# Optimization experiments

Measured on AMD Instinct MI355X. Metric: run time of the kernel, lower is better.

Reference implementation:

```python
import jax, jax.numpy as jnp
import numpy as np

V, E, H, T, B, NT = 50000, 100, 256, 128, 512, 20


def _gl(k, shape, fan):
    return jax.random.normal(k, shape, jnp.float32) * (1.0 / np.sqrt(fan))


def setup_inputs() -> dict:
    key = jax.random.key(0)
    ks = jax.random.split(key, 20)
    inp = {
        'word_inputs': jax.random.randint(ks[0], (B, T), 0, V),
        'word_seq_lengths': jnp.full((B,), T, dtype=jnp.int32),
        'char_inputs': jnp.zeros((B * T, 1), dtype=jnp.int32),
        'batch_label': jax.random.randint(ks[1], (B, T), 0, NT),
        'mask': jnp.ones((B, T), dtype=jnp.bool_),
        'embed': _gl(ks[2], (V, E), E).at[0].set(0.0),  # padding_idx=0
    }
    i = 3
    for d in ('f', 'b'):
        inp['Wih_' + d] = _gl(ks[i + 0], (4 * H, E), E)
        inp['Whh_' + d] = _gl(ks[i + 1], (4 * H, H), H)
        inp['bih_' + d] = jnp.zeros((4 * H,), jnp.float32)
        inp['bhh_' + d] = jnp.zeros((4 * H,), jnp.float32)
        inp['Q_' + d] = _gl(ks[i + 2], (H, E), H)  # mogrify round 1: x <- 2*sig(h Q) * x
        inp['R_' + d] = _gl(ks[i + 3], (E, H), E)  # mogrify round 2: h <- 2*sig(x R) * h
        i += 4
    inp['Wt'] = _gl(ks[i], (NT, 2 * H), 2 * H)
    inp['bt'] = jnp.zeros((NT,), jnp.float32)
    return inp


def _mog_lstm(xs, Wih, Whh, bih, bhh, Q, R):
    # xs: [T, B, E]; mog=2 Mogrifier rounds then standard LSTM cell (i,f,g,o order)
    def step(carry, xt):
        h, c = carry
        xm = 2.0 * jax.nn.sigmoid(h @ Q) * xt
        hm = 2.0 * jax.nn.sigmoid(xm @ R) * h
        g = xm @ Wih.T + hm @ Whh.T + (bih + bhh)
        gi, gf, gg, go = jnp.split(g, 4, axis=-1)
        c = jax.nn.sigmoid(gf) * c + jax.nn.sigmoid(gi) * jnp.tanh(gg)
        h = jax.nn.sigmoid(go) * jnp.tanh(c)
        return (h, c), h
    h0 = jnp.zeros((xs.shape[1], H), xs.dtype)
    _, hs = jax.lax.scan(step, (h0, h0), xs)
    return hs  # [T, B, H]


def reference(word_inputs, word_seq_lengths, char_inputs, batch_label, mask,
              embed, Wih_f, Whh_f, bih_f, bhh_f, Q_f, R_f,
              Wih_b, Whh_b, bih_b, bhh_b, Q_b, R_b, Wt, bt):
    x = embed[word_inputs]                       # [B, T, E]; dropout = identity (eval)
    xs = jnp.transpose(x, (1, 0, 2))             # [T, B, E]
    hf = _mog_lstm(xs, Wih_f, Whh_f, bih_f, bhh_f, Q_f, R_f)
    hb = _mog_lstm(xs[::-1], Wih_b, Whh_b, bih_b, bhh_b, Q_b, R_b)[::-1]
    feat = jnp.concatenate([hf, hb], axis=-1)    # [T, B, 2H]
    logits = feat @ Wt.T + bt                    # [T, B, NT]
    tag_seq = jnp.argmax(logits, axis=-1).T      # [B, T]
    return mask.astype(tag_seq.dtype) * tag_seq
```

## Files before the change

kernel.cpp:

```cpp
#include <hip/hip_runtime.h>
#include <math.h>

#define TT 128
#define BB 512
#define EE 100
#define HH 256
#define G4 1024
#define NTAG 20
#define NCH 92
#define PW3SZ (NCH * 4096)
#define QP2SZ (16 * 1600)
#define RP3SZ (7 * 4096)

__device__ __forceinline__ float sigm(float x) { return 1.0f / (1.0f + expf(-x)); }

__global__ void prep7(const float* __restrict__ Wih, const float* __restrict__ Whh,
                      const float* __restrict__ bih, const float* __restrict__ bhh,
                      const float* __restrict__ Q, const float* __restrict__ R,
                      float* __restrict__ PW3, float* __restrict__ QP2,
                      float* __restrict__ RP3, float* __restrict__ bP)
{
    int idx = blockIdx.x * blockDim.x + threadIdx.x;
    if (idx < PW3SZ) {
        int chunk = idx >> 12, rem = idx & 4095;
        int n = rem >> 2, kk = rem & 3;
        int k = chunk * 4 + kk;
        PW3[idx] = (k < EE) ? Wih[n * EE + k]
                 : (k < EE + HH) ? Whh[n * HH + (k - EE)] : 0.f;
    } else if (idx < PW3SZ + QP2SZ) {
        int i = idx - PW3SZ;
        int kqb = i / 1600, rem = i - kqb * 1600;
        int e = rem >> 4, q = (rem >> 2) & 3, kk = rem & 3;
        int k = (kqb * 4 + q) * 4 + kk;
        QP2[i] = Q[k * EE + e];
    } else if (idx < PW3SZ + QP2SZ + RP3SZ) {
        int i = idx - (PW3SZ + QP2SZ);
        int kqb = i >> 12, rem = i & 4095;
        int j = rem >> 4, q = (rem >> 2) & 3, kk = rem & 3;
        int k = (kqb * 4 + q) * 4 + kk;
        RP3[i] = (k < EE) ? R[k * HH + j] : 0.f;
    } else if (idx < PW3SZ + QP2SZ + RP3SZ + G4) {
        int n = idx - (PW3SZ + QP2SZ + RP3SZ);
        bP[n] = bih[n] + bhh[n];
    }
}

#define P3L(S, c) { const int cc_ = ((c) <= 45) ? (c) : 45; \
    const float* wp_ = PWd + (size_t)(cbase + cc_) * 4096 + n0 * 4; \
    W##S##0 = *(const float4*)(wp_);      W##S##1 = *(const float4*)(wp_ + 4); \
    W##S##2 = *(const float4*)(wp_ + 8);  W##S##3 = *(const float4*)(wp_ + 12); \
    const float* xp_ = sAT + (cbase + cc_) * 16; \
    X##S##0 = *(const float4*)(xp_);      X##S##1 = *(const float4*)(xp_ + 4); \
    X##S##2 = *(const float4*)(xp_ + 8);  X##S##3 = *(const float4*)(xp_ + 12); }

#define P3F(S) { \
    a00 += (X##S##0).x*(W##S##0).x + (X##S##1).x*(W##S##0).y + (X##S##2).x*(W##S##0).z + (X##S##3).x*(W##S##0).w; \
    a01 += (X##S##0).x*(W##S##1).x + (X##S##1).x*(W##S##1).y + (X##S##2).x*(W##S##1).z + (X##S##3).x*(W##S##1).w; \
    a02 += (X##S##0).x*(W##S##2).x + (X##S##1).x*(W##S##2).y + (X##S##2).x*(W##S##2).z + (X##S##3).x*(W##S##2).w; \
    a03 += (X##S##0).x*(W##S##3).x + (X##S##1).x*(W##S##3).y + (X##S##2).x*(W##S##3).z + (X##S##3).x*(W##S##3).w; \
    a10 += (X##S##0).y*(W##S##0).x + (X##S##1).y*(W##S##0).y + (X##S##2).y*(W##S##0).z + (X##S##3).y*(W##S##0).w; \
    a11 += (X##S##0).y*(W##S##1).x + (X##S##1).y*(W##S##1).y + (X##S##2).y*(W##S##1).z + (X##S##3).y*(W##S##1).w; \
    a12 += (X##S##0).y*(W##S##2).x + (X##S##1).y*(W##S##2).y + (X##S##2).y*(W##S##2).z + (X##S##3).y*(W##S##2).w; \
    a13 += (X##S##0).y*(W##S##3).x + (X##S##1).y*(W##S##3).y + (X##S##2).y*(W##S##3).z + (X##S##3).y*(W##S##3).w; \
    a20 += (X##S##0).z*(W##S##0).x + (X##S##1).z*(W##S##0).y + (X##S##2).z*(W##S##0).z + (X##S##3).z*(W##S##0).w; \
    a21 += (X##S##0).z*(W##S##1).x + (X##S##1).z*(W##S##1).y + (X##S##2).z*(W##S##1).z + (X##S##3).z*(W##S##1).w; \
    a22 += (X##S##0).z*(W##S##2).x + (X##S##1).z*(W##S##2).y + (X##S##2).z*(W##S##2).z + (X##S##3).z*(W##S##2).w; \
    a23 += (X##S##0).z*(W##S##3).x + (X##S##1).z*(W##S##3).y + (X##S##2).z*(W##S##3).z + (X##S##3).z*(W##S##3).w; \
    a30 += (X##S##0).w*(W##S##0).x + (X##S##1).w*(W##S##0).y + (X##S##2).w*(W##S##0).z + (X##S##3).w*(W##S##0).w; \
    a31 += (X##S##0).w*(W##S##1).x + (X##S##1).w*(W##S##1).y + (X##S##2).w*(W##S##1).z + (X##S##3).w*(W##S##1).w; \
    a32 += (X##S##0).w*(W##S##2).x + (X##S##1).w*(W##S##2).y + (X##S##2).w*(W##S##2).z + (X##S##3).w*(W##S##2).w; \
    a33 += (X##S##0).w*(W##S##3).x + (X##S##1).w*(W##S##3).y + (X##S##2).w*(W##S##3).z + (X##S##3).w*(W##S##3).w; }

__global__ __launch_bounds__(512, 1) void lstm7(
    const int* __restrict__ words, const float* __restrict__ embed,
    const float* __restrict__ QPf, const float* __restrict__ RPf,
    const float* __restrict__ PWf, const float* __restrict__ bPf,
    const float* __restrict__ QPb, const float* __restrict__ RPb,
    const float* __restrict__ PWb, const float* __restrict__ bPb,
    float* hfbuf, float* hbbuf)
{
    const int bid = blockIdx.x;
    const int dir = bid & 1;
    const int cb  = bid >> 1;
    const int b0  = cb * 4;
    const int tid = threadIdx.x;

    const float* QPd = dir ? QPb : QPf;
    const float* RPd = dir ? RPb : RPf;
    const float* PWd = dir ? PWb : PWf;
    const float* bP  = dir ? bPb : bPf;
    float* hout = dir ? hbbuf : hfbuf;

    __shared__ alignas(16) float sAT[368 * 4];
    __shared__ alignas(16) float sAlin[4 * 112];
    __shared__ alignas(16) float sH[4 * HH];
    __shared__ alignas(16) float sG[2 * 4 * G4];
    __shared__ int sWords[4 * TT];

    const int e  = tid & 127;
    const int r1 = tid >> 7;
    const int j2  = tid & 255;
    const int r20 = (tid >> 8) * 2, r21 = r20 + 1;
    const int n0    = (tid & 255) * 4;
    const int g3    = tid >> 8;
    const int cbase = g3 * 46;
    const int j4  = tid & 255;
    const int r4a = (tid >> 8) * 2, r4b = r4a + 1;
    float c0 = 0.f, c1 = 0.f;

    const float4 bvr = *(const float4*)(bP + n0);
    const float4 bv  = (g3 == 0) ? bvr : make_float4(0.f, 0.f, 0.f, 0.f);

    sWords[tid & 511] = words[(b0 + (tid >> 7)) * TT + (tid & 127)];
    if (tid < 48)  sAT[(356 + (tid >> 2)) * 4 + (tid & 3)] = 0.f;
    if (tid >= 64 && tid < 112) {
        const int i = tid - 64, r = i / 12, p = i - r * 12;
        sAlin[r * 112 + 100 + p] = 0.f;
    }
    __syncthreads();

    for (int s = 0; s < TT; ++s) {
        const int t = dir ? (TT - 1 - s) : s;

        if (e < EE) {
            const int w = sWords[r1 * TT + t];
            const float x = __builtin_nontemporal_load(&embed[(size_t)w * EE + e]);
            if (s == 0) {
                sAT[e * 4 + r1] = x;
                sAlin[r1 * 112 + e] = x;
            } else {
                float ac0 = 0.f, ac1 = 0.f, ac2 = 0.f, ac3 = 0.f;
                const float* hp0 = sH + r1 * HH;
                #pragma unroll
                for (int kqb = 0; kqb < 16; ++kqb) {
                    const float* qp = QPd + kqb * 1600 + e * 16;
                    const float4 q0 = *(const float4*)(qp);
                    const float4 q1 = *(const float4*)(qp + 4);
                    const float4 q2 = *(const float4*)(qp + 8);
                    const float4 q3 = *(const float4*)(qp + 12);
                    const float4 h0 = *(const float4*)(hp0 + kqb * 16);
                    const float4 h1 = *(const float4*)(hp0 + kqb * 16 + 4);
                    const float4 h2 = *(const float4*)(hp0 + kqb * 16 + 8);
                    const float4 h3 = *(const float4*)(hp0 + kqb * 16 + 12);
                    ac0 += h0.x*q0.x + h0.y*q0.y + h0.z*q0.z + h0.w*q0.w;
                    ac1 += h1.x*q1.x + h1.y*q1.y + h1.z*q1.z + h1.w*q1.w;
                    ac2 += h2.x*q2.x + h2.y*q2.y + h2.z*q2.z + h2.w*q2.w;
                    ac3 += h3.x*q3.x + h3.y*q3.y + h3.z*q3.z + h3.w*q3.w;
                }
                const float xm = 2.f * sigm((ac0 + ac1) + (ac2 + ac3)) * x;
                sAT[e * 4 + r1] = xm;
                sAlin[r1 * 112 + e] = xm;
            }
        }
        __syncthreads();

        if (s == 0) {
            sAT[(100 + j2) * 4 + r20] = 0.f;
            sAT[(100 + j2) * 4 + r21] = 0.f;
        } else {
            float s0a = 0.f, s0b = 0.f, s1a = 0.f, s1b = 0.f;
            const float* x0p = sAlin + r20 * 112;
            const float* x1p = sAlin + r21 * 112;
            #pragma unroll
            for (int kqb = 0; kqb < 7; ++kqb) {
                const float* rp = RPd + kqb * 4096 + j2 * 16;
                const float4 w0 = *(const float4*)(rp);
                const float4 w1 = *(const float4*)(rp + 4);
                const float4 w2 = *(const float4*)(rp + 8);
                const float4 w3 = *(const float4*)(rp + 12);
                const float4 xa0 = *(const float4*)(x0p + kqb * 16);
                const float4 xa1 = *(const float4*)(x0p + kqb * 16 + 4);
                const float4 xa2 = *(const float4*)(x0p + kqb * 16 + 8);
                const float4 xa3 = *(const float4*)(x0p + kqb * 16 + 12);
                const float4 xb0 = *(const float4*)(x1p + kqb * 16);
                const float4 xb1 = *(const float4*)(x1p + kqb * 16 + 4);
                const float4 xb2 = *(const float4*)(x1p + kqb * 16 + 8);
                const float4 xb3 = *(const float4*)(x1p + kqb * 16 + 12);
                s0a += xa0.x*w0.x + xa0.y*w0.y + xa0.z*w0.z + xa0.w*w0.w;
                s0b += xa1.x*w1.x + xa1.y*w1.y + xa1.z*w1.z + xa1.w*w1.w;
                s0a += xa2.x*w2.x + xa2.y*w2.y + xa2.z*w2.z + xa2.w*w2.w;
                s0b += xa3.x*w3.x + xa3.y*w3.y + xa3.z*w3.z + xa3.w*w3.w;
                s1a += xb0.x*w0.x + xb0.y*w0.y + xb0.z*w0.z + xb0.w*w0.w;
                s1b += xb1.x*w1.x + xb1.y*w1.y + xb1.z*w1.z + xb1.w*w1.w;
                s1a += xb2.x*w2.x + xb2.y*w2.y + xb2.z*w2.z + xb2.w*w2.w;
                s1b += xb3.x*w3.x + xb3.y*w3.y + xb3.z*w3.z + xb3.w*w3.w;
            }
            sAT[(100 + j2) * 4 + r20] = 2.f * sigm(s0a + s0b) * sH[r20 * HH + j2];
            sAT[(100 + j2) * 4 + r21] = 2.f * sigm(s1a + s1b) * sH[r21 * HH + j2];
        }
        __syncthreads();

        {
            float a00=bv.x,a01=bv.y,a02=bv.z,a03=bv.w;
            float a10=bv.x,a11=bv.y,a12=bv.z,a13=bv.w;
            float a20=bv.x,a21=bv.y,a22=bv.z,a23=bv.w;
            float a30=bv.x,a31=bv.y,a32=bv.z,a33=bv.w;
            float4 WA0,WA1,WA2,WA3,XA0,XA1,XA2,XA3;
            float4 WB0,WB1,WB2,WB3,XB0,XB1,XB2,XB3;
            float4 WC0,WC1,WC2,WC3,XC0,XC1,XC2,XC3;
            P3L(A,0); P3L(B,1); P3L(C,2);
            for (int cc = 0; cc <= 42; cc += 3) {
                P3F(A); P3L(A, cc+3);
                P3F(B); P3L(B, cc+4);
                P3F(C); P3L(C, cc+5);
            }
            P3F(A);
            float* sg = sG + g3 * 4096 + n0;
            *(float4*)(sg)          = make_float4(a00,a01,a02,a03);
            *(float4*)(sg + G4)     = make_float4(a10,a11,a12,a13);
            *(float4*)(sg + 2 * G4) = make_float4(a20,a21,a22,a23);
            *(float4*)(sg + 3 * G4) = make_float4(a30,a31,a32,a33);
        }
        __syncthreads();

        {
            const float* g0 = sG + r4a * G4;
            const float* g1 = sG + r4b * G4;
            const float gi0 = g0[j4]       + g0[4096 + j4];
            const float gf0 = g0[256 + j4] + g0[4096 + 256 + j4];
            const float gg0 = g0[512 + j4] + g0[4096 + 512 + j4];
            const float go0 = g0[768 + j4] + g0[4096 + 768 + j4];
            const float gi1 = g1[j4]       + g1[4096 + j4];
            const float gf1 = g1[256 + j4] + g1[4096 + 256 + j4];
            const float gg1 = g1[512 + j4] + g1[4096 + 512 + j4];
            const float go1 = g1[768 + j4] + g1[4096 + 768 + j4];
            c0 = sigm(gf0) * c0 + sigm(gi0) * tanhf(gg0);
            c1 = sigm(gf1) * c1 + sigm(gi1) * tanhf(gg1);
            const float h0 = sigm(go0) * tanhf(c0);
            const float h1 = sigm(go1) * tanhf(c1);
            sH[r4a * HH + j4] = h0;
            sH[r4b * HH + j4] = h1;
            __builtin_nontemporal_store(h0, &hout[((size_t)t * BB + b0 + r4a) * HH + j4]);
            __builtin_nontemporal_store(h1, &hout[((size_t)t * BB + b0 + r4b) * HH + j4]);
        }
        __syncthreads();
    }
}

__global__ __launch_bounds__(256) void logits_kernel(
    const float* __restrict__ hf, const float* __restrict__ hb,
    const float* __restrict__ Wt, const float* __restrict__ bt,
    int* __restrict__ out)
{
    __shared__ float sW[NTAG][2 * HH];
    __shared__ float sb[NTAG];
    const int tid = threadIdx.x;
    for (int i = tid; i < NTAG * 2 * HH; i += 256) (&sW[0][0])[i] = Wt[i];
    if (tid < NTAG) sb[tid] = bt[tid];
    __syncthreads();

    const int pos = blockIdx.x * 256 + tid;
    const int b  = pos & 511;
    const int t0 = pos >> 9;
    const int t1 = t0 + 64;

    float acc0[NTAG], acc1[NTAG];
    #pragma unroll
    for (int n = 0; n < NTAG; ++n) { acc0[n] = sb[n]; acc1[n] = sb[n]; }

    const float* f0 = hf + ((size_t)t0 * BB + b) * HH;
    const float* f1 = hf + ((size_t)t1 * BB + b) * HH;
    for (int k = 0; k < HH; k += 4) {
        const float4 a0 = *(const float4*)(f0 + k);
        const float4 a1 = *(const float4*)(f1 + k);
        #pragma unroll
        for (int n = 0; n < NTAG; ++n) {
            const float4 w = *(const float4*)&sW[n][k];
            acc0[n] += a0.x * w.x + a0.y * w.y + a0.z * w.z + a0.w * w.w;
            acc1[n] += a1.x * w.x + a1.y * w.y + a1.z * w.z + a1.w * w.w;
        }
    }
    const float* g0 = hb + ((size_t)t0 * BB + b) * HH;
    const float* g1 = hb + ((size_t)t1 * BB + b) * HH;
    for (int k = 0; k < HH; k += 4) {
        const float4 a0 = *(const float4*)(g0 + k);
        const float4 a1 = *(const float4*)(g1 + k);
        #pragma unroll
        for (int n = 0; n < NTAG; ++n) {
            const float4 w = *(const float4*)&sW[n][HH + k];
            acc0[n] += a0.x * w.x + a0.y * w.y + a0.z * w.z + a0.w * w.w;
            acc1[n] += a1.x * w.x + a1.y * w.y + a1.z * w.z + a1.w * w.w;
        }
    }

    float b0v = acc0[0]; int i0 = 0;
    float b1v = acc1[0]; int i1 = 0;
    #pragma unroll
    for (int n = 1; n < NTAG; ++n) {
        if (acc0[n] > b0v) { b0v = acc0[n]; i0 = n; }
        if (acc1[n] > b1v) { b1v = acc1[n]; i1 = n; }
    }
    out[b * TT + t0] = i0;
    out[b * TT + t1] = i1;
}

extern "C" void kernel_launch(void* const* d_in, const int* in_sizes, int n_in,
                              void* d_out, int out_size, void* d_ws, size_t ws_size,
                              hipStream_t stream)
{
    (void)in_sizes; (void)n_in; (void)out_size; (void)ws_size;

    const int*   words = (const int*)  d_in[0];
    const float* embd  = (const float*)d_in[5];
    const float* Wih_f = (const float*)d_in[6];
    const float* Whh_f = (const float*)d_in[7];
    const float* bih_f = (const float*)d_in[8];
    const float* bhh_f = (const float*)d_in[9];
    const float* Q_f   = (const float*)d_in[10];
    const float* R_f   = (const float*)d_in[11];
    const float* Wih_b = (const float*)d_in[12];
    const float* Whh_b = (const float*)d_in[13];
    const float* bih_b = (const float*)d_in[14];
    const float* bhh_b = (const float*)d_in[15];
    const float* Q_b   = (const float*)d_in[16];
    const float* R_b   = (const float*)d_in[17];
    const float* Wt    = (const float*)d_in[18];
    const float* bt    = (const float*)d_in[19];
    int* out = (int*)d_out;

    float* ws   = (float*)d_ws;
    float* PW_f = ws;
    float* QP_f = PW_f + PW3SZ;
    float* RP_f = QP_f + QP2SZ;
    float* bP_f = RP_f + RP3SZ;
    float* PW_b = bP_f + G4;
    float* QP_b = PW_b + PW3SZ;
    float* RP_b = QP_b + QP2SZ;
    float* bP_b = RP_b + RP3SZ;
    float* hf   = bP_b + G4;
    float* hb   = hf + (size_t)TT * BB * HH;

    const int prep_grid = (PW3SZ + QP2SZ + RP3SZ + G4 + 255) / 256;
    prep7<<<prep_grid, 256, 0, stream>>>(Wih_f, Whh_f, bih_f, bhh_f, Q_f, R_f,
                                         PW_f, QP_f, RP_f, bP_f);
    prep7<<<prep_grid, 256, 0, stream>>>(Wih_b, Whh_b, bih_b, bhh_b, Q_b, R_b,
                                         PW_b, QP_b, RP_b, bP_b);
    lstm7<<<256, 512, 0, stream>>>(words, embd, QP_f, RP_f, PW_f, bP_f,
                                   QP_b, RP_b, PW_b, bP_b, hf, hb);
    logits_kernel<<<128, 256, 0, stream>>>(hf, hb, Wt, bt, out);
}
```

Baseline: 4.157 ms.

## Split LSTM blocks to two batch rows each and drop K-split gate reduction

The recurrent kernel now uses 512 blocks of 256 threads, each handling 2 batch rows instead of 4, with two blocks per CU allowed. The gate GEMM loses the two-way K split: each thread covers all 92 weight chunks for its 4 gate columns, with a 4-stage register pipeline, and the partial-sum reduction in shared memory goes away. The aim is more blocks in flight, fewer threads per barrier and less shared-memory traffic. The cost is that every gate weight chunk is read from global/L2 for only 2 batch rows instead of 4, doubling total weight traffic, and the per-thread serial loop is twice as long.

```diff
diff --git a/kernel.cpp b/kernel.cpp
--- a/kernel.cpp
+++ b/kernel.cpp
@@ -45,33 +45,24 @@
     }
 }
 
-#define P3L(S, c) { const int cc_ = ((c) <= 45) ? (c) : 45; \
-    const float* wp_ = PWd + (size_t)(cbase + cc_) * 4096 + n0 * 4; \
+#define P3L(S, c) { \
+    const float* wp_ = PWd + (size_t)(c) * 4096 + n0 * 4; \
     W##S##0 = *(const float4*)(wp_);      W##S##1 = *(const float4*)(wp_ + 4); \
     W##S##2 = *(const float4*)(wp_ + 8);  W##S##3 = *(const float4*)(wp_ + 12); \
-    const float* xp_ = sAT + (cbase + cc_) * 16; \
-    X##S##0 = *(const float4*)(xp_);      X##S##1 = *(const float4*)(xp_ + 4); \
-    X##S##2 = *(const float4*)(xp_ + 8);  X##S##3 = *(const float4*)(xp_ + 12); }
+    const float* xp_ = sAT + (c) * 8; \
+    X##S##a = *(const float4*)(xp_);      X##S##b = *(const float4*)(xp_ + 4); }
 
 #define P3F(S) { \
-    a00 += (X##S##0).x*(W##S##0).x + (X##S##1).x*(W##S##0).y + (X##S##2).x*(W##S##0).z + (X##S##3).x*(W##S##0).w; \
-    a01 += (X##S##0).x*(W##S##1).x + (X##S##1).x*(W##S##1).y + (X##S##2).x*(W##S##1).z + (X##S##3).x*(W##S##1).w; \
-    a02 += (X##S##0).x*(W##S##2).x + (X##S##1).x*(W##S##2).y + (X##S##2).x*(W##S##2).z + (X##S##3).x*(W##S##2).w; \
-    a03 += (X##S##0).x*(W##S##3).x + (X##S##1).x*(W##S##3).y + (X##S##2).x*(W##S##3).z + (X##S##3).x*(W##S##3).w; \
-    a10 += (X##S##0).y*(W##S##0).x + (X##S##1).y*(W##S##0).y + (X##S##2).y*(W##S##0).z + (X##S##3).y*(W##S##0).w; \
-    a11 += (X##S##0).y*(W##S##1).x + (X##S##1).y*(W##S##1).y + (X##S##2).y*(W##S##1).z + (X##S##3).y*(W##S##1).w; \
-    a12 += (X##S##0).y*(W##S##2).x + (X##S##1).y*(W##S##2).y + (X##S##2).y*(W##S##2).z + (X##S##3).y*(W##S##2).w; \
-    a13 += (X##S##0).y*(W##S##3).x + (X##S##1).y*(W##S##3).y + (X##S##2).y*(W##S##3).z + (X##S##3).y*(W##S##3).w; \
-    a20 += (X##S##0).z*(W##S##0).x + (X##S##1).z*(W##S##0).y + (X##S##2).z*(W##S##0).z + (X##S##3).z*(W##S##0).w; \
-    a21 += (X##S##0).z*(W##S##1).x + (X##S##1).z*(W##S##1).y + (X##S##2).z*(W##S##1).z + (X##S##3).z*(W##S##1).w; \
-    a22 += (X##S##0).z*(W##S##2).x + (X##S##1).z*(W##S##2).y + (X##S##2).z*(W##S##2).z + (X##S##3).z*(W##S##2).w; \
-    a23 += (X##S##0).z*(W##S##3).x + (X##S##1).z*(W##S##3).y + (X##S##2).z*(W##S##3).z + (X##S##3).z*(W##S##3).w; \
-    a30 += (X##S##0).w*(W##S##0).x + (X##S##1).w*(W##S##0).y + (X##S##2).w*(W##S##0).z + (X##S##3).w*(W##S##0).w; \
-    a31 += (X##S##0).w*(W##S##1).x + (X##S##1).w*(W##S##1).y + (X##S##2).w*(W##S##1).z + (X##S##3).w*(W##S##1).w; \
-    a32 += (X##S##0).w*(W##S##2).x + (X##S##1).w*(W##S##2).y + (X##S##2).w*(W##S##2).z + (X##S##3).w*(W##S##2).w; \
-    a33 += (X##S##0).w*(W##S##3).x + (X##S##1).w*(W##S##3).y + (X##S##2).w*(W##S##3).z + (X##S##3).w*(W##S##3).w; }
-
-__global__ __launch_bounds__(512, 1) void lstm7(
+    a00 += (X##S##a).x*(W##S##0).x + (X##S##a).z*(W##S##0).y + (X##S##b).x*(W##S##0).z + (X##S##b).z*(W##S##0).w; \
+    a01 += (X##S##a).x*(W##S##1).x + (X##S##a).z*(W##S##1).y + (X##S##b).x*(W##S##1).z + (X##S##b).z*(W##S##1).w; \
+    a02 += (X##S##a).x*(W##S##2).x + (X##S##a).z*(W##S##2).y + (X##S##b).x*(W##S##2).z + (X##S##b).z*(W##S##2).w; \
+    a03 += (X##S##a).x*(W##S##3).x + (X##S##a).z*(W##S##3).y + (X##S##b).x*(W##S##3).z + (X##S##b).z*(W##S##3).w; \
+    a10 += (X##S##a).y*(W##S##0).x + (X##S##a).w*(W##S##0).y + (X##S##b).y*(W##S##0).z + (X##S##b).w*(W##S##0).w; \
+    a11 += (X##S##a).y*(W##S##1).x + (X##S##a).w*(W##S##1).y + (X##S##b).y*(W##S##1).z + (X##S##b).w*(W##S##1).w; \
+    a12 += (X##S##a).y*(W##S##2).x + (X##S##a).w*(W##S##2).y + (X##S##b).y*(W##S##2).z + (X##S##b).w*(W##S##2).w; \
+    a13 += (X##S##a).y*(W##S##3).x + (X##S##a).w*(W##S##3).y + (X##S##b).y*(W##S##3).z + (X##S##b).w*(W##S##3).w; }
+
+__global__ __launch_bounds__(256, 2) void lstm8(
     const int* __restrict__ words, const float* __restrict__ embed,
     const float* __restrict__ QPf, const float* __restrict__ RPf,
     const float* __restrict__ PWf, const float* __restrict__ bPf,
@@ -82,7 +73,7 @@
     const int bid = blockIdx.x;
     const int dir = bid & 1;
     const int cb  = bid >> 1;
-    const int b0  = cb * 4;
+    const int b0  = cb * 2;
     const int tid = threadIdx.x;
 
     const float* QPd = dir ? QPb : QPf;
@@ -91,30 +82,24 @@
     const float* bP  = dir ? bPb : bPf;
     float* hout = dir ? hbbuf : hfbuf;
 
-    __shared__ alignas(16) float sAT[368 * 4];
-    __shared__ alignas(16) float sAlin[4 * 112];
-    __shared__ alignas(16) float sH[4 * HH];
-    __shared__ alignas(16) float sG[2 * 4 * G4];
-    __shared__ int sWords[4 * TT];
+    __shared__ alignas(16) float sAT[368 * 2];
+    __shared__ alignas(16) float sAlin[2 * 112];
+    __shared__ alignas(16) float sH[2 * HH];
+    __shared__ alignas(16) float sG[2 * G4];
+    __shared__ int sWords[2 * TT];
 
     const int e  = tid & 127;
     const int r1 = tid >> 7;
-    const int j2  = tid & 255;
-    const int r20 = (tid >> 8) * 2, r21 = r20 + 1;
-    const int n0    = (tid & 255) * 4;
-    const int g3    = tid >> 8;
-    const int cbase = g3 * 46;
-    const int j4  = tid & 255;
-    const int r4a = (tid >> 8) * 2, r4b = r4a + 1;
+    const int j2 = tid;
+    const int n0 = tid * 4;
     float c0 = 0.f, c1 = 0.f;
 
-    const float4 bvr = *(const float4*)(bP + n0);
-    const float4 bv  = (g3 == 0) ? bvr : make_float4(0.f, 0.f, 0.f, 0.f);
-
-    sWords[tid & 511] = words[(b0 + (tid >> 7)) * TT + (tid & 127)];
-    if (tid < 48)  sAT[(356 + (tid >> 2)) * 4 + (tid & 3)] = 0.f;
-    if (tid >= 64 && tid < 112) {
-        const int i = tid - 64, r = i / 12, p = i - r * 12;
+    const float4 bv = *(const float4*)(bP + n0);
+
+    sWords[tid] = words[(b0 + (tid >> 7)) * TT + (tid & 127)];
+    if (tid < 24) sAT[(356 + (tid >> 1)) * 2 + (tid & 1)] = 0.f;
+    if (tid >= 32 && tid < 56) {
+        const int i = tid - 32, r = i / 12, p = i - r * 12;
         sAlin[r * 112 + 100 + p] = 0.f;
     }
     __syncthreads();
@@ -126,7 +111,7 @@
             const int w = sWords[r1 * TT + t];
             const float x = __builtin_nontemporal_load(&embed[(size_t)w * EE + e]);
             if (s == 0) {
-                sAT[e * 4 + r1] = x;
+                sAT[e * 2 + r1] = x;
                 sAlin[r1 * 112 + e] = x;
             } else {
                 float ac0 = 0.f, ac1 = 0.f, ac2 = 0.f, ac3 = 0.f;
@@ -148,19 +133,19 @@
                     ac3 += h3.x*q3.x + h3.y*q3.y + h3.z*q3.z + h3.w*q3.w;
                 }
                 const float xm = 2.f * sigm((ac0 + ac1) + (ac2 + ac3)) * x;
-                sAT[e * 4 + r1] = xm;
+                sAT[e * 2 + r1] = xm;
                 sAlin[r1 * 112 + e] = xm;
             }
         }
         __syncthreads();
 
         if (s == 0) {
-            sAT[(100 + j2) * 4 + r20] = 0.f;
-            sAT[(100 + j2) * 4 + r21] = 0.f;
+            sAT[(100 + j2) * 2 + 0] = 0.f;
+            sAT[(100 + j2) * 2 + 1] = 0.f;
         } else {
             float s0a = 0.f, s0b = 0.f, s1a = 0.f, s1b = 0.f;
-            const float* x0p = sAlin + r20 * 112;
-            const float* x1p = sAlin + r21 * 112;
+            const float* x0p = sAlin;
+            const float* x1p = sAlin + 112;
             #pragma unroll
             for (int kqb = 0; kqb < 7; ++kqb) {
                 const float* rp = RPd + kqb * 4096 + j2 * 16;
@@ -185,53 +170,44 @@
                 s1a += xb2.x*w2.x + xb2.y*w2.y + xb2.z*w2.z + xb2.w*w2.w;
                 s1b += xb3.x*w3.x + xb3.y*w3.y + xb3.z*w3.z + xb3.w*w3.w;
             }
-            sAT[(100 + j2) * 4 + r20] = 2.f * sigm(s0a + s0b) * sH[r20 * HH + j2];
-            sAT[(100 + j2) * 4 + r21] = 2.f * sigm(s1a + s1b) * sH[r21 * HH + j2];
+            sAT[(100 + j2) * 2 + 0] = 2.f * sigm(s0a + s0b) * sH[j2];
+            sAT[(100 + j2) * 2 + 1] = 2.f * sigm(s1a + s1b) * sH[HH + j2];
         }
         __syncthreads();
 
         {
             float a00=bv.x,a01=bv.y,a02=bv.z,a03=bv.w;
             float a10=bv.x,a11=bv.y,a12=bv.z,a13=bv.w;
-            float a20=bv.x,a21=bv.y,a22=bv.z,a23=bv.w;
-            float a30=bv.x,a31=bv.y,a32=bv.z,a33=bv.w;
-            float4 WA0,WA1,WA2,WA3,XA0,XA1,XA2,XA3;
-            float4 WB0,WB1,WB2,WB3,XB0,XB1,XB2,XB3;
-            float4 WC0,WC1,WC2,WC3,XC0,XC1,XC2,XC3;
-            P3L(A,0); P3L(B,1); P3L(C,2);
-            for (int cc = 0; cc <= 42; cc += 3) {
-                P3F(A); P3L(A, cc+3);
-                P3F(B); P3L(B, cc+4);
-                P3F(C); P3L(C, cc+5);
+            float4 WA0,WA1,WA2,WA3,XAa,XAb;
+            float4 WB0,WB1,WB2,WB3,XBa,XBb;
+            float4 WC0,WC1,WC2,WC3,XCa,XCb;
+            float4 WD0,WD1,WD2,WD3,XDa,XDb;
+            P3L(A,0); P3L(B,1); P3L(C,2); P3L(D,3);
+            for (int cc = 0; cc <= 84; cc += 4) {
+                P3F(A); P3L(A, cc+4);
+                P3F(B); P3L(B, cc+5);
+                P3F(C); P3L(C, cc+6);
+                P3F(D); P3L(D, cc+7);
             }
-            P3F(A);
-            float* sg = sG + g3 * 4096 + n0;
-            *(float4*)(sg)          = make_float4(a00,a01,a02,a03);
-            *(float4*)(sg + G4)     = make_float4(a10,a11,a12,a13);
-            *(float4*)(sg + 2 * G4) = make_float4(a20,a21,a22,a23);
-            *(float4*)(sg + 3 * G4) = make_float4(a30,a31,a32,a33);
+            P3F(A); P3F(B); P3F(C); P3F(D);
+            *(float4*)(sG + n0)      = make_float4(a00,a01,a02,a03);
+            *(float4*)(sG + G4 + n0) = make_float4(a10,a11,a12,a13);
         }
         __syncthreads();
 
         {
-            const float* g0 = sG + r4a * G4;
-            const float* g1 = sG + r4b * G4;
-            const float gi0 = g0[j4]       + g0[4096 + j4];
-            const float gf0 = g0[256 + j4] + g0[4096 + 256 + j4];
-            const float gg0 = g0[512 + j4] + g0[4096 + 512 + j4];
-            const float go0 = g0[768 + j4] + g0[4096 + 768 + j4];
-            const float gi1 = g1[j4]       + g1[4096 + j4];
-            const float gf1 = g1[256 + j4] + g1[4096 + 256 + j4];
-            const float gg1 = g1[512 + j4] + g1[4096 + 512 + j4];
-            const float go1 = g1[768 + j4] + g1[4096 + 768 + j4];
+            const float gi0 = sG[j2],       gi1 = sG[G4 + j2];
+            const float gf0 = sG[256 + j2], gf1 = sG[G4 + 256 + j2];
+            const float gg0 = sG[512 + j2], gg1 = sG[G4 + 512 + j2];
+            const float go0 = sG[768 + j2], go1 = sG[G4 + 768 + j2];
             c0 = sigm(gf0) * c0 + sigm(gi0) * tanhf(gg0);
             c1 = sigm(gf1) * c1 + sigm(gi1) * tanhf(gg1);
             const float h0 = sigm(go0) * tanhf(c0);
             const float h1 = sigm(go1) * tanhf(c1);
-            sH[r4a * HH + j4] = h0;
-            sH[r4b * HH + j4] = h1;
-            __builtin_nontemporal_store(h0, &hout[((size_t)t * BB + b0 + r4a) * HH + j4]);
-            __builtin_nontemporal_store(h1, &hout[((size_t)t * BB + b0 + r4b) * HH + j4]);
+            sH[j2]      = h0;
+            sH[HH + j2] = h1;
+            __builtin_nontemporal_store(h0, &hout[((size_t)t * BB + b0 + 0) * HH + j2]);
+            __builtin_nontemporal_store(h1, &hout[((size_t)t * BB + b0 + 1) * HH + j2]);
         }
         __syncthreads();
     }
@@ -335,7 +311,7 @@
                                          PW_f, QP_f, RP_f, bP_f);
     prep7<<<prep_grid, 256, 0, stream>>>(Wih_b, Whh_b, bih_b, bhh_b, Q_b, R_b,
                                          PW_b, QP_b, RP_b, bP_b);
-    lstm7<<<256, 512, 0, stream>>>(words, embd, QP_f, RP_f, PW_f, bP_f,
+    lstm8<<<512, 256, 0, stream>>>(words, embd, QP_f, RP_f, PW_f, bP_f,
                                    QP_b, RP_b, PW_b, bP_b, hf, hb);
     logits_kernel<<<128, 256, 0, stream>>>(hf, hb, Wt, bt, out);
 }
```

New measurement: 6.779 ms. 1.63x slower.

## Double LSTM block size to 1024 threads, splitting gate GEMM K into four slices

Applied to the files above, without the earlier changes.

The recurrent kernel now runs 1024 threads per block instead of 512. The fused gate GEMM splits its K dimension into four groups of 23 chunks rather than two of 46, and the R-mogrify and cell-update stages each handle one batch row per thread instead of two. Partial gate sums go to a padded shared buffer with a row stride of 1028 to reduce bank conflicts, and are reduced across four slices. The goal is to shorten each serial timestep by spreading its work over more waves, at the cost of more registers per thread pressure limits, a larger shared footprint, and extra reduction reads.

```diff
diff --git a/kernel.cpp b/kernel.cpp
--- a/kernel.cpp
+++ b/kernel.cpp
@@ -11,6 +11,8 @@
 #define PW3SZ (NCH * 4096)
 #define QP2SZ (16 * 1600)
 #define RP3SZ (7 * 4096)
+#define SGR 1028
+#define SGG (4 * SGR)
 
 __device__ __forceinline__ float sigm(float x) { return 1.0f / (1.0f + expf(-x)); }
 
@@ -45,7 +47,7 @@
     }
 }
 
-#define P3L(S, c) { const int cc_ = ((c) <= 45) ? (c) : 45; \
+#define P3L(S, c) { const int cc_ = ((c) <= 22) ? (c) : 22; \
     const float* wp_ = PWd + (size_t)(cbase + cc_) * 4096 + n0 * 4; \
     W##S##0 = *(const float4*)(wp_);      W##S##1 = *(const float4*)(wp_ + 4); \
     W##S##2 = *(const float4*)(wp_ + 8);  W##S##3 = *(const float4*)(wp_ + 12); \
@@ -71,7 +73,7 @@
     a32 += (X##S##0).w*(W##S##2).x + (X##S##1).w*(W##S##2).y + (X##S##2).w*(W##S##2).z + (X##S##3).w*(W##S##2).w; \
     a33 += (X##S##0).w*(W##S##3).x + (X##S##1).w*(W##S##3).y + (X##S##2).w*(W##S##3).z + (X##S##3).w*(W##S##3).w; }
 
-__global__ __launch_bounds__(512, 1) void lstm7(
+__global__ __launch_bounds__(1024) void lstm9(
     const int* __restrict__ words, const float* __restrict__ embed,
     const float* __restrict__ QPf, const float* __restrict__ RPf,
     const float* __restrict__ PWf, const float* __restrict__ bPf,
@@ -94,24 +96,24 @@
     __shared__ alignas(16) float sAT[368 * 4];
     __shared__ alignas(16) float sAlin[4 * 112];
     __shared__ alignas(16) float sH[4 * HH];
-    __shared__ alignas(16) float sG[2 * 4 * G4];
+    __shared__ alignas(16) float sG[4 * SGG];
     __shared__ int sWords[4 * TT];
 
     const int e  = tid & 127;
-    const int r1 = tid >> 7;
-    const int j2  = tid & 255;
-    const int r20 = (tid >> 8) * 2, r21 = r20 + 1;
+    const int r1 = (tid >> 7) & 3;
+    const int j2 = tid & 255;
+    const int r2 = tid >> 8;
     const int n0    = (tid & 255) * 4;
     const int g3    = tid >> 8;
-    const int cbase = g3 * 46;
-    const int j4  = tid & 255;
-    const int r4a = (tid >> 8) * 2, r4b = r4a + 1;
-    float c0 = 0.f, c1 = 0.f;
+    const int cbase = g3 * 23;
+    const int j4 = tid & 255;
+    const int r4 = tid >> 8;
+    float c0 = 0.f;
 
     const float4 bvr = *(const float4*)(bP + n0);
     const float4 bv  = (g3 == 0) ? bvr : make_float4(0.f, 0.f, 0.f, 0.f);
 
-    sWords[tid & 511] = words[(b0 + (tid >> 7)) * TT + (tid & 127)];
+    if (tid < 512) sWords[tid] = words[(b0 + (tid >> 7)) * TT + (tid & 127)];
     if (tid < 48)  sAT[(356 + (tid >> 2)) * 4 + (tid & 3)] = 0.f;
     if (tid >= 64 && tid < 112) {
         const int i = tid - 64, r = i / 12, p = i - r * 12;
@@ -122,7 +124,7 @@
     for (int s = 0; s < TT; ++s) {
         const int t = dir ? (TT - 1 - s) : s;
 
-        if (e < EE) {
+        if (tid < 512 && e < EE) {
             const int w = sWords[r1 * TT + t];
             const float x = __builtin_nontemporal_load(&embed[(size_t)w * EE + e]);
             if (s == 0) {
@@ -155,12 +157,10 @@
         __syncthreads();
 
         if (s == 0) {
-            sAT[(100 + j2) * 4 + r20] = 0.f;
-            sAT[(100 + j2) * 4 + r21] = 0.f;
+            sAT[(100 + j2) * 4 + r2] = 0.f;
         } else {
-            float s0a = 0.f, s0b = 0.f, s1a = 0.f, s1b = 0.f;
-            const float* x0p = sAlin + r20 * 112;
-            const float* x1p = sAlin + r21 * 112;
+            float sa = 0.f, sb = 0.f;
+            const float* xp = sAlin + r2 * 112;
             #pragma unroll
             for (int kqb = 0; kqb < 7; ++kqb) {
                 const float* rp = RPd + kqb * 4096 + j2 * 16;
@@ -168,25 +168,16 @@
                 const float4 w1 = *(const float4*)(rp + 4);
                 const float4 w2 = *(const float4*)(rp + 8);
                 const float4 w3 = *(const float4*)(rp + 12);
-                const float4 xa0 = *(const float4*)(x0p + kqb * 16);
-                const float4 xa1 = *(const float4*)(x0p + kqb * 16 + 4);
-                const float4 xa2 = *(const float4*)(x0p + kqb * 16 + 8);
-                const float4 xa3 = *(const float4*)(x0p + kqb * 16 + 12);
-                const float4 xb0 = *(const float4*)(x1p + kqb * 16);
-                const float4 xb1 = *(const float4*)(x1p + kqb * 16 + 4);
-                const float4 xb2 = *(const float4*)(x1p + kqb * 16 + 8);
-                const float4 xb3 = *(const float4*)(x1p + kqb * 16 + 12);
-                s0a += xa0.x*w0.x + xa0.y*w0.y + xa0.z*w0.z + xa0.w*w0.w;
-                s0b += xa1.x*w1.x + xa1.y*w1.y + xa1.z*w1.z + xa1.w*w1.w;
-                s0a += xa2.x*w2.x + xa2.y*w2.y + xa2.z*w2.z + xa2.w*w2.w;
-                s0b += xa3.x*w3.x + xa3.y*w3.y + xa3.z*w3.z + xa3.w*w3.w;
-                s1a += xb0.x*w0.x + xb0.y*w0.y + xb0.z*w0.z + xb0.w*w0.w;
-                s1b += xb1.x*w1.x + xb1.y*w1.y + xb1.z*w1.z + xb1.w*w1.w;
-                s1a += xb2.x*w2.x + xb2.y*w2.y + xb2.z*w2.z + xb2.w*w2.w;
-                s1b += xb3.x*w3.x + xb3.y*w3.y + xb3.z*w3.z + xb3.w*w3.w;
+                const float4 x0 = *(const float4*)(xp + kqb * 16);
+                const float4 x1 = *(const float4*)(xp + kqb * 16 + 4);
+                const float4 x2 = *(const float4*)(xp + kqb * 16 + 8);
+                const float4 x3 = *(const float4*)(xp + kqb * 16 + 12);
+                sa += x0.x*w0.x + x0.y*w0.y + x0.z*w0.z + x0.w*w0.w;
+                sb += x1.x*w1.x + x1.y*w1.y + x1.z*w1.z + x1.w*w1.w;
+                sa += x2.x*w2.x + x2.y*w2.y + x2.z*w2.z + x2.w*w2.w;
+                sb += x3.x*w3.x + x3.y*w3.y + x3.z*w3.z + x3.w*w3.w;
             }
-            sAT[(100 + j2) * 4 + r20] = 2.f * sigm(s0a + s0b) * sH[r20 * HH + j2];
-            sAT[(100 + j2) * 4 + r21] = 2.f * sigm(s1a + s1b) * sH[r21 * HH + j2];
+            sAT[(100 + j2) * 4 + r2] = 2.f * sigm(sa + sb) * sH[r2 * HH + j2];
         }
         __syncthreads();
 
@@ -197,41 +188,30 @@
             float a30=bv.x,a31=bv.y,a32=bv.z,a33=bv.w;
             float4 WA0,WA1,WA2,WA3,XA0,XA1,XA2,XA3;
             float4 WB0,WB1,WB2,WB3,XB0,XB1,XB2,XB3;
-            float4 WC0,WC1,WC2,WC3,XC0,XC1,XC2,XC3;
-            P3L(A,0); P3L(B,1); P3L(C,2);
-            for (int cc = 0; cc <= 42; cc += 3) {
-                P3F(A); P3L(A, cc+3);
-                P3F(B); P3L(B, cc+4);
-                P3F(C); P3L(C, cc+5);
+            P3L(A,0); P3L(B,1);
+            for (int cc = 0; cc <= 20; cc += 2) {
+                P3F(A); P3L(A, cc+2);
+                P3F(B); P3L(B, cc+3);
             }
             P3F(A);
-            float* sg = sG + g3 * 4096 + n0;
-            *(float4*)(sg)          = make_float4(a00,a01,a02,a03);
-            *(float4*)(sg + G4)     = make_float4(a10,a11,a12,a13);
-            *(float4*)(sg + 2 * G4) = make_float4(a20,a21,a22,a23);
-            *(float4*)(sg + 3 * G4) = make_float4(a30,a31,a32,a33);
+            float* sg = sG + g3 * SGG + n0;
+            *(float4*)(sg)           = make_float4(a00,a01,a02,a03);
+            *(float4*)(sg + SGR)     = make_float4(a10,a11,a12,a13);
+            *(float4*)(sg + 2 * SGR) = make_float4(a20,a21,a22,a23);
+            *(float4*)(sg + 3 * SGR) = make_float4(a30,a31,a32,a33);
         }
         __syncthreads();
 
         {
-            const float* g0 = sG + r4a * G4;
-            const float* g1 = sG + r4b * G4;
-            const float gi0 = g0[j4]       + g0[4096 + j4];
-            const float gf0 = g0[256 + j4] + g0[4096 + 256 + j4];
-            const float gg0 = g0[512 + j4] + g0[4096 + 512 + j4];
-            const float go0 = g0[768 + j4] + g0[4096 + 768 + j4];
-            const float gi1 = g1[j4]       + g1[4096 + j4];
-            const float gf1 = g1[256 + j4] + g1[4096 + 256 + j4];
-            const float gg1 = g1[512 + j4] + g1[4096 + 512 + j4];
-            const float go1 = g1[768 + j4] + g1[4096 + 768 + j4];
-            c0 = sigm(gf0) * c0 + sigm(gi0) * tanhf(gg0);
-            c1 = sigm(gf1) * c1 + sigm(gi1) * tanhf(gg1);
-            const float h0 = sigm(go0) * tanhf(c0);
-            const float h1 = sigm(go1) * tanhf(c1);
-            sH[r4a * HH + j4] = h0;
-            sH[r4b * HH + j4] = h1;
-            __builtin_nontemporal_store(h0, &hout[((size_t)t * BB + b0 + r4a) * HH + j4]);
-            __builtin_nontemporal_store(h1, &hout[((size_t)t * BB + b0 + r4b) * HH + j4]);
+            const float* g = sG + r4 * SGR;
+            const float gi = g[j4]       + g[SGG + j4]       + g[2*SGG + j4]       + g[3*SGG + j4];
+            const float gf = g[256 + j4] + g[SGG + 256 + j4] + g[2*SGG + 256 + j4] + g[3*SGG + 256 + j4];
+            const float gg = g[512 + j4] + g[SGG + 512 + j4] + g[2*SGG + 512 + j4] + g[3*SGG + 512 + j4];
+            const float go = g[768 + j4] + g[SGG + 768 + j4] + g[2*SGG + 768 + j4] + g[3*SGG + 768 + j4];
+            c0 = sigm(gf) * c0 + sigm(gi) * tanhf(gg);
+            const float hv = sigm(go) * tanhf(c0);
+            sH[r4 * HH + j4] = hv;
+            __builtin_nontemporal_store(hv, &hout[((size_t)t * BB + b0 + r4) * HH + j4]);
         }
         __syncthreads();
     }
@@ -335,7 +315,7 @@
                                          PW_f, QP_f, RP_f, bP_f);
     prep7<<<prep_grid, 256, 0, stream>>>(Wih_b, Whh_b, bih_b, bhh_b, Q_b, R_b,
                                          PW_b, QP_b, RP_b, bP_b);
-    lstm7<<<256, 512, 0, stream>>>(words, embd, QP_f, RP_f, PW_f, bP_f,
-                                   QP_b, RP_b, PW_b, bP_b, hf, hb);
+    lstm9<<<256, 1024, 0, stream>>>(words, embd, QP_f, RP_f, PW_f, bP_f,
+                                    QP_b, RP_b, PW_b, bP_b, hf, hb);
     logits_kernel<<<128, 256, 0, stream>>>(hf, hb, Wt, bt, out);
 }
```

After: 5.360 ms. 1.29x slower.
